# Kernel tuning notes

Measured on AMD Instinct MI355X. Metric: run time of the kernel, lower is better.

Reference implementation:

```python
import jax, jax.numpy as jnp
import numpy as np

N_ANCH = 100800   # 3 * (160^2 + 80^2 + 40^2), YOLOv5 @ 1280
NUM_CLS = 80
IMG_HW = 1280
MAX_DETS = 300    # fixed padding for jit-compatible NMS output
OUT = 224
SCORE_THRESH = 0.1
IOU_THRESH = 0.45
ALLOWED = jnp.array([1, 2, 3, 4, 6, 8, 17, 18, 44], dtype=jnp.int32)
MEAN = jnp.array([0.485, 0.456, 0.406], dtype=jnp.float32).reshape(1, 3, 1, 1)
STD = jnp.array([0.229, 0.224, 0.225], dtype=jnp.float32).reshape(1, 3, 1, 1)


def setup_inputs() -> dict:
    key = jax.random.key(0)
    k1, k2, k3, k4, k5 = jax.random.split(key, 5)
    # realistic YOLO-style raw predictions: cx,cy in-image, modest w,h, gaussian class logits
    cxcy = jax.random.uniform(k1, (1, 2, N_ANCH), dtype=jnp.float32) * IMG_HW
    wh = jax.random.uniform(k2, (1, 2, N_ANCH), dtype=jnp.float32) * 256.0 + 8.0
    obj = jax.random.uniform(k3, (1, 1, N_ANCH), dtype=jnp.float32)
    logits = jax.random.normal(k4, (1, NUM_CLS, N_ANCH), dtype=jnp.float32)
    raw_pred = jnp.concatenate([cxcy, wh, obj, logits], axis=1)  # [1, 5+C, N]
    image = jax.random.uniform(k5, (1, 3, IMG_HW, IMG_HW), dtype=jnp.float32)
    return {"raw_pred": raw_pred, "image": image}


def _pairwise_iou(b):
    # b: [K,4] xyxy
    area = (b[:, 2] - b[:, 0]) * (b[:, 3] - b[:, 1])
    lt = jnp.maximum(b[:, None, :2], b[None, :, :2])
    rb = jnp.minimum(b[:, None, 2:], b[None, :, 2:])
    wh = jnp.clip(rb - lt, 0.0)
    inter = wh[..., 0] * wh[..., 1]
    union = area[:, None] + area[None, :] - inter
    return inter / jnp.maximum(union, 1e-9)


def _nms_keep(iou, valid):
    # greedy NMS over score-sorted boxes; returns boolean keep mask [K]
    K = iou.shape[0]
    idx = jnp.arange(K)

    def body(i, keep):
        suppress = keep[i] & (iou[i] > IOU_THRESH) & (idx > i)
        return keep & ~suppress

    return jax.lax.fori_loop(0, K, body, valid)


def _roi_align(image_chw, boxes):
    # torchvision roi_align, aligned=True, one sample per bin at the bin center
    # (sampling_ratio fixed to 1; see notes). image_chw: [3,H,W], boxes: [M,4]
    C, H, W = image_chw.shape
    grid = (jnp.arange(OUT, dtype=jnp.float32) + 0.5) / OUT  # fractional bin centers

    def one(box):
        x1, y1, x2, y2 = box
        xs = x1 - 0.5 + grid * (x2 - x1)  # [OUT], aligned=True half-pixel offset
        ys = y1 - 0.5 + grid * (y2 - y1)
        vx = (xs >= -1.0) & (xs <= W)
        vy = (ys >= -1.0) & (ys <= H)
        xc = jnp.clip(xs, 0.0, W - 1)
        yc = jnp.clip(ys, 0.0, H - 1)
        x0 = jnp.floor(xc).astype(jnp.int32)
        y0 = jnp.floor(yc).astype(jnp.int32)
        x1i = jnp.minimum(x0 + 1, W - 1)
        y1i = jnp.minimum(y0 + 1, H - 1)
        lx = xc - x0
        ly = yc - y0
        # bilinear gather: [3, OUT, OUT]
        v00 = image_chw[:, y0[:, None], x0[None, :]]
        v01 = image_chw[:, y0[:, None], x1i[None, :]]
        v10 = image_chw[:, y1i[:, None], x0[None, :]]
        v11 = image_chw[:, y1i[:, None], x1i[None, :]]
        top = v00 * (1.0 - lx) + v01 * lx
        bot = v10 * (1.0 - lx) + v11 * lx
        val = top * (1.0 - ly)[None, :, None] + bot * ly[None, :, None]
        return jnp.where(vy[None, :, None] & vx[None, None, :], val, 0.0)

    return jax.vmap(one)(boxes)


def _forward(raw_pred, image):
    x = raw_pred[0].T  # [N, 5+C]
    cx, cy, w, h = x[:, 0], x[:, 1], x[:, 2], x[:, 3]
    boxes = jnp.stack([cx - w / 2, cy - h / 2, cx + w / 2, cy + h / 2], axis=1)
    cls_logits = x[:, 5:]
    scores = cls_logits.max(axis=1)
    classes = cls_logits.argmax(axis=1).astype(jnp.int32) + 1
    # score + allowed-class filter (mask form)
    mask = (scores > SCORE_THRESH) & jnp.isin(classes, ALLOWED)
    masked_scores = jnp.where(mask, scores, jnp.finfo(scores.dtype).min)
    top_scores, top_idx = jax.lax.top_k(masked_scores, MAX_DETS)  # sorted desc
    top_boxes = boxes[top_idx]
    top_classes = classes[top_idx]
    valid = mask[top_idx]
    # greedy NMS over padded top-K candidates
    keep = _nms_keep(_pairwise_iou(top_boxes), valid)
    final_boxes = jnp.where(keep[:, None], top_boxes, 0.0)
    final_scores = jnp.where(keep, top_scores, 0.0)
    final_classes = jnp.where(keep, top_classes, 0)
    # crops: full image first, then RoIAlign crops, normalized once
    full_crop = jax.image.resize(image, (1, 3, OUT, OUT), method='linear', antialias=False)
    roi_crops = _roi_align(image[0], final_boxes)  # [K,3,224,224]
    roi_crops = jnp.where(keep[:, None, None, None], roi_crops, 0.0)
    all_crops = jnp.concatenate([full_crop, roi_crops], axis=0)  # [K+1,3,224,224]
    all_crops = (all_crops - MEAN) / STD
    return final_boxes, final_scores, final_classes, all_crops, keep


def reference(raw_pred, image):
    return _forward(raw_pred, image)
```

## Files before the change

### kernel.cpp

```cpp
#include <hip/hip_runtime.h>
#include <stdint.h>

#define N_ANCH   100800
#define NUM_CLS  80
#define IMG_HW   1280
#define MAX_DETS 300
#define OUTSZ    224
#define CAND_CAP 4096
#define LIST_CAP 16384

#define OFF_BOXES   0
#define OFF_SCORES  1200
#define OFF_CLASSES 1500
#define OFF_CROPS   1800
#define CROPS_ELEMS (301 * 3 * 224 * 224)
#define OFF_KEEP    (OFF_CROPS + CROPS_ELEMS)

#define SC_CNT    0
#define SC_CAND   64

typedef float f32x4 __attribute__((ext_vector_type(4)));

__device__ __forceinline__ uint32_t fkey(float f) {
    uint32_t u = __float_as_uint(f);
    return (u & 0x80000000u) ? ~u : (u | 0x80000000u);
}
__device__ __forceinline__ float unfkey(uint32_t k) {
    uint32_t u = (k & 0x80000000u) ? (k & 0x7fffffffu) : ~k;
    return __uint_as_float(u);
}

__global__ void k_score(const float* __restrict__ rp,
                        unsigned long long* __restrict__ cand,
                        uint32_t* __restrict__ cnt) {
    int gid = blockIdx.x * 256 + threadIdx.x;
    int grp = gid >> 3;
    int cp  = gid & 7;
    bool in = (grp < N_ANCH / 4);
    int a4 = in ? grp * 4 : 0;

    float best[4] = {-3.402823466e38f, -3.402823466e38f, -3.402823466e38f, -3.402823466e38f};
    int   bc[4]   = {0, 0, 0, 0};
    #pragma unroll
    for (int k = 0; k < 10; ++k) {
        int c = cp + 8 * k;
        float4 v = *(const float4*)&rp[(size_t)(5 + c) * N_ANCH + a4];
        if (v.x > best[0]) { best[0] = v.x; bc[0] = c; }
        if (v.y > best[1]) { best[1] = v.y; bc[1] = c; }
        if (v.z > best[2]) { best[2] = v.z; bc[2] = c; }
        if (v.w > best[3]) { best[3] = v.w; bc[3] = c; }
    }
    #pragma unroll
    for (int m = 1; m < 8; m <<= 1) {
        #pragma unroll
        for (int j = 0; j < 4; ++j) {
            float ob = __shfl_xor(best[j], m);
            int   oc = __shfl_xor(bc[j], m);
            if (ob > best[j] || (ob == best[j] && oc < bc[j])) { best[j] = ob; bc[j] = oc; }
        }
    }

    const unsigned long long AM =
        (1ULL << 1) | (1ULL << 2) | (1ULL << 3) | (1ULL << 4) | (1ULL << 6) |
        (1ULL << 8) | (1ULL << 17) | (1ULL << 18) | (1ULL << 44);
    unsigned long long pk[4];
    int cnt_loc = 0;
    bool lead = (cp == 0) && in;
    #pragma unroll
    for (int k = 0; k < 4; ++k) {
        int cls = bc[k] + 1;
        bool mk = lead && (best[k] > 0.1f) && (cls < 64) && ((AM >> cls) & 1ULL);
        uint32_t low = ((0x1FFFFu ^ (uint32_t)(a4 + k)) << 7) | (uint32_t)cls;
        pk[k] = mk ? (((unsigned long long)fkey(best[k]) << 32) | low) : 0ull;
        cnt_loc += mk ? 1 : 0;
    }

    int inc = cnt_loc;
    #pragma unroll
    for (int d = 1; d < 64; d <<= 1) {
        int vv = __shfl_up(inc, d);
        if ((threadIdx.x & 63) >= d) inc += vv;
    }
    int total = __shfl(inc, 63);
    uint32_t base = 0u;
    if (((threadIdx.x & 63) == 63) && total > 0) base = atomicAdd(cnt, (uint32_t)total);
    base = (uint32_t)__shfl((int)base, 63);
    uint32_t pos = base + (uint32_t)(inc - cnt_loc);
    #pragma unroll
    for (int k = 0; k < 4; ++k) {
        if (pk[k]) {
            if (pos < LIST_CAP) cand[pos] = pk[k];
            ++pos;
        }
    }
}

__global__ void __launch_bounds__(1024) k_detect(const float* __restrict__ rp,
                                                 const unsigned long long* __restrict__ cand,
                                                 const uint32_t* __restrict__ cnt_p,
                                                 float* __restrict__ out) {
    __shared__ uint32_t lhist[16384];
    __shared__ uint32_t ssum[1024];
    __shared__ uint32_t swave[16];
    __shared__ int      sh_thr;
    __shared__ uint32_t s_cnt;
    __shared__ unsigned long long sb[CAND_CAP];
    __shared__ unsigned long long top[MAX_DETS];
    __shared__ float sbx[MAX_DETS][4];
    __shared__ float sscore[MAX_DETS];
    __shared__ int   scls[MAX_DETS];
    __shared__ __align__(8) uint32_t sup[MAX_DETS][10];
    __shared__ __align__(8) uint32_t kw[10];
    __shared__ __align__(8) uint32_t rnz[10];
    int t = threadIdx.x;
    int nl = min((int)(*cnt_p), LIST_CAP);

    #pragma unroll
    for (int i = 0; i < 16; ++i) lhist[t + i * 1024] = 0u;
    if (t == 0) s_cnt = 0u;
    __syncthreads();
    for (int i = t; i < nl; i += 1024)
        atomicAdd(&lhist[(uint32_t)(cand[i] >> 50)], 1u);
    __syncthreads();

    const uint4* h4 = (const uint4*)(&lhist[t * 16]);
    uint4 v0 = h4[0], v1 = h4[1], v2 = h4[2], v3 = h4[3];
    uint32_t s = v0.x + v0.y + v0.z + v0.w + v1.x + v1.y + v1.z + v1.w +
                 v2.x + v2.y + v2.z + v2.w + v3.x + v3.y + v3.z + v3.w;
    ssum[t] = s;
    uint32_t ws = s;
    #pragma unroll
    for (int m = 32; m; m >>= 1) ws += __shfl_xor(ws, m);
    if ((t & 63) == 0) swave[t >> 6] = ws;
    __syncthreads();
    if (t == 0) {
        uint32_t acc = 0; int wsel = -1;
        for (int w = 15; w >= 0; --w) {
            uint32_t v = swave[w];
            if (acc + v >= (uint32_t)MAX_DETS) { wsel = w; break; }
            acc += v;
        }
        int thr = 0;
        if (wsel >= 0) {
            int tsel = -1;
            for (int tg = wsel * 64 + 63; tg >= wsel * 64; --tg) {
                uint32_t v = ssum[tg];
                if (acc + v >= (uint32_t)MAX_DETS) { tsel = tg; break; }
                acc += v;
            }
            for (int b = tsel * 16 + 15; b >= tsel * 16; --b) {
                acc += lhist[b];
                if (acc >= (uint32_t)MAX_DETS) { thr = b; break; }
            }
        }
        sh_thr = thr;
    }
    __syncthreads();

    uint32_t thr = (uint32_t)sh_thr;
    for (int i = t; i < nl; i += 1024) {
        unsigned long long key = cand[i];
        if ((uint32_t)(key >> 50) >= thr) {
            uint32_t pos = atomicAdd(&s_cnt, 1u);
            if (pos < CAND_CAP) sb[pos] = key;
        }
    }
    __syncthreads();
    int n = min((int)s_cnt, CAND_CAP);

    if (t < MAX_DETS) top[t] = 0ull;
    for (int i = t; i < MAX_DETS * 10; i += 1024) ((uint32_t*)sup)[i] = 0u;
    if (t < 10) { kw[t] = 0u; rnz[t] = 0u; }
    __syncthreads();

    for (int i = t; i < n; i += 1024) {
        unsigned long long key = sb[i];
        int rank = 0;
        for (int j = 0; j < n; ++j) rank += (sb[j] > key) ? 1 : 0;
        if (rank < MAX_DETS) top[rank] = key;
    }
    __syncthreads();

    if (t < MAX_DETS) {
        unsigned long long key = top[t];
        bool valid = (key != 0ull);
        float score = 0.f; int cls = 0;
        float b0 = 0.f, b1 = 0.f, b2 = 0.f, b3 = 0.f;
        if (valid) {
            uint32_t low = (uint32_t)key;
            uint32_t a = 0x1FFFFu ^ ((low >> 7) & 0x1FFFFu);
            cls = (int)(low & 0x7Fu);
            score = unfkey((uint32_t)(key >> 32));
            float cx = rp[a], cy = rp[N_ANCH + a];
            float w = rp[2 * N_ANCH + a], h = rp[3 * N_ANCH + a];
            b0 = cx - w * 0.5f; b1 = cy - h * 0.5f;
            b2 = cx + w * 0.5f; b3 = cy + h * 0.5f;
            atomicOr(&kw[t >> 5], 1u << (t & 31));
        }
        sbx[t][0] = b0; sbx[t][1] = b1; sbx[t][2] = b2; sbx[t][3] = b3;
        sscore[t] = score; scls[t] = cls;
    }
    __syncthreads();

    for (int p = t; p < MAX_DETS * MAX_DETS; p += 1024) {
        int i = p / MAX_DETS, j = p % MAX_DETS;
        if (j > i) {
            float ax1 = sbx[i][0], ay1 = sbx[i][1], ax2 = sbx[i][2], ay2 = sbx[i][3];
            float bx1 = sbx[j][0], by1 = sbx[j][1], bx2 = sbx[j][2], by2 = sbx[j][3];
            float areaA = (ax2 - ax1) * (ay2 - ay1);
            float areaB = (bx2 - bx1) * (by2 - by1);
            float ltx = fmaxf(ax1, bx1), lty = fmaxf(ay1, by1);
            float rbx = fminf(ax2, bx2), rby = fminf(ay2, by2);
            float iw = fmaxf(rbx - ltx, 0.f), ih = fmaxf(rby - lty, 0.f);
            float inter = iw * ih;
            float uni = areaA + areaB - inter;
            float iou = inter / fmaxf(uni, 1e-9f);
            if (iou > 0.45f) {
                atomicOr(&sup[i][j >> 5], 1u << (j & 31));
                atomicOr(&rnz[i >> 5], 1u << (i & 31));
            }
        }
    }
    __syncthreads();

    if (t == 0) {
        unsigned long long kwr[5], rnzr[5];
        const unsigned long long* kq = (const unsigned long long*)kw;
        const unsigned long long* rq = (const unsigned long long*)rnz;
        #pragma unroll
        for (int w = 0; w < 5; ++w) { kwr[w] = kq[w]; rnzr[w] = rq[w]; }
        #pragma unroll
        for (int sblk = 0; sblk < 5; ++sblk) {
            int lim = (sblk == 4) ? (MAX_DETS - 4 * 64) : 64;
            for (int i2 = 0; i2 < lim; ++i2) {
                if (((kwr[sblk] >> i2) & 1ull) && ((rnzr[sblk] >> i2) & 1ull)) {
                    int i = sblk * 64 + i2;
                    const unsigned long long* row = (const unsigned long long*)&sup[i][0];
                    kwr[0] &= ~row[0]; kwr[1] &= ~row[1]; kwr[2] &= ~row[2];
                    kwr[3] &= ~row[3]; kwr[4] &= ~row[4];
                }
            }
        }
        unsigned long long* kqo = (unsigned long long*)kw;
        #pragma unroll
        for (int w = 0; w < 5; ++w) kqo[w] = kwr[w];
    }
    __syncthreads();

    if (t < MAX_DETS) {
        bool kp = (kw[t >> 5] >> (t & 31)) & 1u;
        out[OFF_BOXES + t * 4 + 0] = kp ? sbx[t][0] : 0.f;
        out[OFF_BOXES + t * 4 + 1] = kp ? sbx[t][1] : 0.f;
        out[OFF_BOXES + t * 4 + 2] = kp ? sbx[t][2] : 0.f;
        out[OFF_BOXES + t * 4 + 3] = kp ? sbx[t][3] : 0.f;
        out[OFF_SCORES + t]  = kp ? sscore[t] : 0.f;
        out[OFF_CLASSES + t] = kp ? (float)scls[t] : 0.f;
        out[OFF_KEEP + t]    = kp ? 1.f : 0.f;
    }
}

#define TROWS  8
#define TPITCH 272

__global__ void k_crops(const float* __restrict__ img, float* __restrict__ out) {
    __shared__ float tile[TROWS * TPITCH];
    int bx = blockIdx.x;
    int n  = blockIdx.y;
    int t = threadIdx.x;
    int q = bx * 256 + t;
    int oy = q / 56;
    int ox0 = (q - oy * 56) * 4;
    const float scl[3] = {1.0f / 0.229f, 1.0f / 0.224f, 1.0f / 0.225f};
    const float bia[3] = {-0.485f / 0.229f, -0.456f / 0.224f, -0.406f / 0.225f};
    size_t obase = (size_t)OFF_CROPS + (size_t)(n * 3) * (OUTSZ * OUTSZ)
                 + (size_t)oy * OUTSZ + ox0;

    if (n == 0) {
        float sy = ((float)oy + 0.5f) * (1280.0f / 224.0f) - 0.5f;
        int y0 = (int)floorf(sy);
        float ly = sy - (float)y0;
        int x0a[4]; float lxa[4];
        #pragma unroll
        for (int k = 0; k < 4; ++k) {
            float sx = ((float)(ox0 + k) + 0.5f) * (1280.0f / 224.0f) - 0.5f;
            x0a[k] = (int)floorf(sx);
            lxa[k] = sx - floorf(sx);
        }
        #pragma unroll
        for (int c = 0; c < 3; ++c) {
            const float* r0 = img + (size_t)c * (IMG_HW * IMG_HW) + (size_t)y0 * IMG_HW;
            const float* r1 = r0 + IMG_HW;
            f32x4 v;
            #pragma unroll
            for (int k = 0; k < 4; ++k) {
                float t00 = r0[x0a[k]], t01 = r0[x0a[k] + 1];
                float t10 = r1[x0a[k]], t11 = r1[x0a[k] + 1];
                float top = __builtin_fmaf(lxa[k], t01 - t00, t00);
                float bot = __builtin_fmaf(lxa[k], t11 - t10, t10);
                float val = __builtin_fmaf(ly, bot - top, top);
                v[k] = __builtin_fmaf(val, scl[c], bia[c]);
            }
            __builtin_nontemporal_store(v, (f32x4*)(out + obase + (size_t)c * (OUTSZ * OUTSZ)));
        }
        return;
    }

    float kp = out[OFF_KEEP + (n - 1)];
    if (kp == 0.f) {
        #pragma unroll
        for (int c = 0; c < 3; ++c) {
            f32x4 v = (f32x4){bia[c], bia[c], bia[c], bia[c]};
            __builtin_nontemporal_store(v, (f32x4*)(out + obase + (size_t)c * (OUTSZ * OUTSZ)));
        }
        return;
    }

    float4 bxv = *(const float4*)&out[OFF_BOXES + (n - 1) * 4];
    float x1b = bxv.x, y1b = bxv.y, x2b = bxv.z, y2b = bxv.w;
    float bw = x2b - x1b, bh = y2b - y1b;
    float x1bm = x1b - 0.5f, y1bm = y1b - 0.5f;
    int oy_s = (bx * 256) / 56;
    int oy_e = (bx * 256 + 255) / 56;
    float ys0 = y1bm + (((float)oy_s + 0.5f) / 224.0f) * bh;
    float ys1 = y1bm + (((float)oy_e + 0.5f) / 224.0f) * bh;
    float xs0 = x1bm + (0.5f / 224.0f) * bw;
    float xs1 = x1bm + (223.5f / 224.0f) * bw;
    int iy_min = (int)floorf(fminf(fmaxf(ys0, 0.f), 1279.f));
    int iy_max = min((int)floorf(fminf(fmaxf(ys1, 0.f), 1279.f)) + 1, IMG_HW - 1);
    int ix_min = (int)floorf(fminf(fmaxf(xs0, 0.f), 1279.f));
    int ix_max = min((int)floorf(fminf(fmaxf(xs1, 0.f), 1279.f)) + 1, IMG_HW - 1);
    int ix_al = ix_min & ~3;
    int rows = iy_max - iy_min + 1;
    int w4   = (ix_max - ix_al + 4) >> 2;
    int total = rows * w4;
    float winv = 1.0f / (float)w4;

    float gy = ((float)oy + 0.5f) / 224.0f;
    float ys = y1bm + gy * bh;
    bool vy = (ys >= -1.0f) && (ys <= 1280.0f);
    float ycl = fminf(fmaxf(ys, 0.f), 1279.f);
    int y0 = (int)floorf(ycl);
    int y1i = min(y0 + 1, IMG_HW - 1);
    float ly = ycl - (float)y0;
    int rb0 = (y0 - iy_min) * TPITCH - ix_al;
    int rb1 = (y1i - iy_min) * TPITCH - ix_al;
    int a0a[4], a1a[4];
    int d1a[4];
    float lxa[4]; bool oka[4];
    #pragma unroll
    for (int k = 0; k < 4; ++k) {
        float gx = ((float)(ox0 + k) + 0.5f) / 224.0f;
        float xs = x1bm + gx * bw;
        oka[k] = vy && (xs >= -1.0f) && (xs <= 1280.0f);
        float xcl = fminf(fmaxf(xs, 0.f), 1279.f);
        int x0 = (int)floorf(xcl);
        int x1i = min(x0 + 1, IMG_HW - 1);
        lxa[k] = xcl - (float)x0;
        a0a[k] = rb0 + x0;
        a1a[k] = rb1 + x0;
        d1a[k] = x1i - x0;
    }

    for (int c = 0; c < 3; ++c) {
        if (c) __syncthreads();
        const float* ch = img + (size_t)c * (IMG_HW * IMG_HW);
        for (int i = t; i < total; i += 256) {
            int r  = (int)((float)i * winv);
            int cc = i - r * w4;
            if (cc < 0)        { r--; cc += w4; }
            else if (cc >= w4) { r++; cc -= w4; }
            int gyr = iy_min + r;
            int px = ix_al + cc * 4;
            const float* src = ch + (size_t)gyr * IMG_HW + px;
            float4 val;
            if ((px + 3 < IMG_HW) || (gyr < IMG_HW - 1) || (c < 2)) {
                val = *(const float4*)src;
            } else {
                val.x = src[0];
                val.y = src[min(1, IMG_HW - 1 - px)];
                val.z = src[min(2, IMG_HW - 1 - px)];
                val.w = src[min(3, IMG_HW - 1 - px)];
            }
            *(float4*)&tile[r * TPITCH + cc * 4] = val;
        }
        __syncthreads();
        f32x4 v;
        #pragma unroll
        for (int k = 0; k < 4; ++k) {
            float t00 = tile[a0a[k]], t01 = tile[a0a[k] + d1a[k]];
            float t10 = tile[a1a[k]], t11 = tile[a1a[k] + d1a[k]];
            float top = __builtin_fmaf(lxa[k], t01 - t00, t00);
            float bot = __builtin_fmaf(lxa[k], t11 - t10, t10);
            float val = __builtin_fmaf(ly, bot - top, top);
            if (!oka[k]) val = 0.f;
            v[k] = __builtin_fmaf(val, scl[c], bia[c]);
        }
        __builtin_nontemporal_store(v, (f32x4*)(out + obase + (size_t)c * (OUTSZ * OUTSZ)));
    }
}

extern "C" void kernel_launch(void* const* d_in, const int* in_sizes, int n_in,
                              void* d_out, int out_size, void* d_ws, size_t ws_size,
                              hipStream_t stream) {
    (void)in_sizes; (void)n_in; (void)out_size; (void)d_ws; (void)ws_size;
    const float* rp  = (const float*)d_in[0];
    const float* img = (const float*)d_in[1];
    float* out = (float*)d_out;
    char* sbase = (char*)d_out + (size_t)OFF_CROPS * sizeof(float);
    uint32_t* cnt = (uint32_t*)(sbase + SC_CNT);
    unsigned long long* cand = (unsigned long long*)(sbase + SC_CAND);

    hipMemsetAsync(sbase, 0, 64, stream);
    k_score<<<(N_ANCH / 4 * 8 + 255) / 256, 256, 0, stream>>>(rp, cand, cnt);
    k_detect<<<1, 1024, 0, stream>>>(rp, cand, cnt, out);
    dim3 grid(49, 301);
    k_crops<<<grid, 256, 0, stream>>>(img, out);
}
```

Baseline: 327.0 us.

## Double-buffer RoI crop tile staging across channels with precomputed load addresses

The RoI crop kernel now holds two shared-memory tiles and stages the next channel's image rows while the current channel is interpolated. This removes one barrier per channel and lets global loads overlap the LDS reads and stores. The per-thread source and destination offsets are computed once, assuming at most three float4 loads per thread, instead of being recomputed per channel. Right-edge clamping now works by copying the last pixel into a padding slot, so the x1-x0 delta array is dropped. This doubles the shared-memory footprint and assumes total never exceeds 768.

Measured after the change: 324.1 us. About the same (-0.9%).

```diff
diff --git a/kernel.cpp b/kernel.cpp
--- a/kernel.cpp
+++ b/kernel.cpp
@@ -261,9 +261,10 @@
 
 #define TROWS  8
 #define TPITCH 272
+#define TSIZE  (TROWS * TPITCH)
 
 __global__ void k_crops(const float* __restrict__ img, float* __restrict__ out) {
-    __shared__ float tile[TROWS * TPITCH];
+    __shared__ float tile[2][TSIZE + 4];
     int bx = blockIdx.x;
     int n  = blockIdx.y;
     int t = threadIdx.x;
@@ -334,6 +335,25 @@
     int w4   = (ix_max - ix_al + 4) >> 2;
     int total = rows * w4;
     float winv = 1.0f / (float)w4;
+    int D = (IMG_HW - 1) - ix_al;
+    bool rep = (ix_max == IMG_HW - 1);
+
+    int soff[3], doff[3], px3[3]; bool sval[3], safe4[3];
+    #pragma unroll
+    for (int s = 0; s < 3; ++s) {
+        int i = t + s * 256;
+        sval[s] = (i < total);
+        int r  = (int)((float)i * winv);
+        int cc = i - r * w4;
+        if (cc < 0)        { r--; cc += w4; }
+        else if (cc >= w4) { r++; cc -= w4; }
+        int gyr = iy_min + r;
+        int px = ix_al + cc * 4;
+        soff[s]  = gyr * IMG_HW + px;
+        doff[s]  = r * TPITCH + cc * 4;
+        safe4[s] = (px + 3 < IMG_HW) || (gyr < IMG_HW - 1);
+        px3[s]   = IMG_HW - 1 - px;
+    }
 
     float gy = ((float)oy + 0.5f) / 224.0f;
     float ys = y1bm + gy * bh;
@@ -344,9 +364,7 @@
     float ly = ycl - (float)y0;
     int rb0 = (y0 - iy_min) * TPITCH - ix_al;
     int rb1 = (y1i - iy_min) * TPITCH - ix_al;
-    int a0a[4], a1a[4];
-    int d1a[4];
-    float lxa[4]; bool oka[4];
+    int a0a[4], a1a[4]; float lxa[4]; bool oka[4];
     #pragma unroll
     for (int k = 0; k < 4; ++k) {
         float gx = ((float)(ox0 + k) + 0.5f) / 224.0f;
@@ -354,41 +372,46 @@
         oka[k] = vy && (xs >= -1.0f) && (xs <= 1280.0f);
         float xcl = fminf(fmaxf(xs, 0.f), 1279.f);
         int x0 = (int)floorf(xcl);
-        int x1i = min(x0 + 1, IMG_HW - 1);
         lxa[k] = xcl - (float)x0;
         a0a[k] = rb0 + x0;
         a1a[k] = rb1 + x0;
-        d1a[k] = x1i - x0;
-    }
-
+    }
+
+    auto stage = [&](float* __restrict__ tb, int c) {
+        const float* __restrict__ ch = img + (size_t)c * (IMG_HW * IMG_HW);
+        #pragma unroll
+        for (int s = 0; s < 3; ++s) {
+            if (sval[s]) {
+                const float* src = ch + soff[s];
+                float4 val;
+                if (safe4[s] || c < 2) {
+                    val = *(const float4*)src;
+                } else {
+                    val.x = src[0];
+                    val.y = src[min(1, px3[s])];
+                    val.z = src[min(2, px3[s])];
+                    val.w = src[min(3, px3[s])];
+                }
+                *(float4*)&tb[doff[s]] = val;
+            }
+        }
+        if (rep) {
+            for (int r2 = t; r2 < rows; r2 += 256)
+                tb[r2 * TPITCH + D + 1] = ch[(size_t)(iy_min + r2) * IMG_HW + (IMG_HW - 1)];
+        }
+    };
+
+    stage(tile[0], 0);
+    __syncthreads();
+    #pragma unroll
     for (int c = 0; c < 3; ++c) {
-        if (c) __syncthreads();
-        const float* ch = img + (size_t)c * (IMG_HW * IMG_HW);
-        for (int i = t; i < total; i += 256) {
-            int r  = (int)((float)i * winv);
-            int cc = i - r * w4;
-            if (cc < 0)        { r--; cc += w4; }
-            else if (cc >= w4) { r++; cc -= w4; }
-            int gyr = iy_min + r;
-            int px = ix_al + cc * 4;
-            const float* src = ch + (size_t)gyr * IMG_HW + px;
-            float4 val;
-            if ((px + 3 < IMG_HW) || (gyr < IMG_HW - 1) || (c < 2)) {
-                val = *(const float4*)src;
-            } else {
-                val.x = src[0];
-                val.y = src[min(1, IMG_HW - 1 - px)];
-                val.z = src[min(2, IMG_HW - 1 - px)];
-                val.w = src[min(3, IMG_HW - 1 - px)];
-            }
-            *(float4*)&tile[r * TPITCH + cc * 4] = val;
-        }
-        __syncthreads();
+        if (c < 2) stage(tile[(c + 1) & 1], c + 1);
+        const float* __restrict__ tb = tile[c & 1];
         f32x4 v;
         #pragma unroll
         for (int k = 0; k < 4; ++k) {
-            float t00 = tile[a0a[k]], t01 = tile[a0a[k] + d1a[k]];
-            float t10 = tile[a1a[k]], t11 = tile[a1a[k] + d1a[k]];
+            float t00 = tb[a0a[k]], t01 = tb[a0a[k] + 1];
+            float t10 = tb[a1a[k]], t11 = tb[a1a[k] + 1];
             float top = __builtin_fmaf(lxa[k], t01 - t00, t00);
             float bot = __builtin_fmaf(lxa[k], t11 - t10, t10);
             float val = __builtin_fmaf(ly, bot - top, top);
@@ -396,6 +419,7 @@
             v[k] = __builtin_fmaf(val, scl[c], bia[c]);
         }
         __builtin_nontemporal_store(v, (f32x4*)(out + obase + (size_t)c * (OUTSZ * OUTSZ)));
+        if (c < 2) __syncthreads();
     }
 }
 
```
